# Kernel optimization log

Hardware: AMD Instinct MI355X
Metric: run time of the kernel (lower is better)

The kernel has to match this reference:

```python
import jax, jax.numpy as jnp
import numpy as np

B, T, S, H = 16, 1024, 1024, 512  # batch, dec len, src len, hidden


def setup_inputs() -> dict:
    key = jax.random.key(0)
    k1, k2, k3, k4 = jax.random.split(key, 4)
    decoder_output = jax.random.normal(k1, (B, T, H), dtype=jnp.float32)
    context = jax.random.normal(k2, (B, S, 2 * H), dtype=jnp.float32)
    mask = jax.random.randint(k3, (B, T, S), 0, 2) > 0  # bool
    # nn.Linear(2H, H, bias=False) weight: [H, 2H]
    W_a = jax.random.normal(k4, (H, 2 * H), dtype=jnp.float32) * (1.0 / np.sqrt(2 * H))
    return {"decoder_output": decoder_output, "context": context, "mask": mask, "W_a": W_a}


def reference(decoder_output, context, mask, W_a):
    # context_in = W_a(context).transpose(1, 2): [B, H, S]
    context_in = jnp.einsum('bsc,hc->bhs', context, W_a)
    # scores: [B, T, S]
    scores = jnp.einsum('bth,bhs->bts', decoder_output, context_in)
    scores = jnp.where(mask, jnp.float32(-1000000.0), scores)
    attn = jax.nn.softmax(scores, axis=2)
    # weighted sum over source: [B, T, 2H]
    weighted_sum = jnp.einsum('bts,bsc->btc', attn, context)
    return weighted_sum
```

## Files before the change

kernel.cpp:

```cpp
#include <hip/hip_runtime.h>
#include <cstdint>
#include <cstddef>


constexpr int BB = 16;
constexpr int TT = 1024;
constexpr int SS = 1024;
constexpr int HH = 512;

typedef __attribute__((ext_vector_type(8))) short short8v;
typedef __attribute__((ext_vector_type(4))) float f32x4;

__device__ inline unsigned short f2bf(float x) {
    unsigned int u = __float_as_uint(x);
    return (unsigned short)((u + 0x7FFFu + ((u >> 16) & 1u)) >> 16);
}
__device__ inline float bf2f(unsigned short h) {
    return __uint_as_float(((unsigned int)h) << 16);
}

__device__ inline void gload16(const void* g, void* l) {
    __builtin_amdgcn_global_load_lds(
        (const __attribute__((address_space(1))) unsigned int*)g,
        (__attribute__((address_space(3))) unsigned int*)l, 16, 0, 0);
}

__global__ __launch_bounds__(256)
void detect_mask(const unsigned char* __restrict__ mask, int* __restrict__ flag) {
    __shared__ int cnt;
    if (threadIdx.x == 0) cnt = 0;
    __syncthreads();
    int c = 0;
    for (int i = threadIdx.x; i < 4096; i += 256)
        if ((i & 3) != 0 && mask[i] != 0) c++;
    atomicAdd(&cnt, c);
    __syncthreads();
    if (threadIdx.x == 0) *flag = (cnt > 0) ? 1 : 0;
}

__global__ __launch_bounds__(256)
void split_hl(const float* __restrict__ in, unsigned short* __restrict__ oh,
              unsigned short* __restrict__ ol)
{
    const size_t i = ((size_t)blockIdx.x * 256 + threadIdx.x) * 8;
    const float4 x = *(const float4*)(in + i);
    const float4 y = *(const float4*)(in + i + 4);
    const float v[8] = {x.x, x.y, x.z, x.w, y.x, y.y, y.z, y.w};
    short8v H, L;
    #pragma unroll
    for (int j = 0; j < 8; ++j) {
        const unsigned short h = f2bf(v[j]);
        H[j] = (short)h;
        L[j] = (short)f2bf(v[j] - bf2f(h));
    }
    *(short8v*)(oh + i) = H;
    *(short8v*)(ol + i) = L;
}

__global__ __launch_bounds__(256)
void transpose_bf16(const float* __restrict__ src, unsigned short* __restrict__ dst,
                    long sS, long sD)
{
    __shared__ float t[32][33];
    const float*    s = src + (long)blockIdx.z * sS;
    unsigned short* d = dst + (long)blockIdx.z * sD;
    const int r0 = blockIdx.x << 5, c0 = blockIdx.y << 5;
    const int x = threadIdx.x & 31, y = threadIdx.x >> 5;
    #pragma unroll
    for (int i = 0; i < 32; i += 8)
        t[y + i][x] = s[(long)(r0 + y + i) * 1024 + c0 + x];
    __syncthreads();
    #pragma unroll
    for (int i = 0; i < 32; i += 8)
        d[(long)(c0 + y + i) * 1024 + r0 + x] = f2bf(t[x][y + i]);
}

template <bool SPLIT>
__global__ __launch_bounds__(256, 2)
void gemm_x3(const unsigned short* __restrict__ Ah, const unsigned short* __restrict__ Al,
             const unsigned short* __restrict__ Bh, const unsigned short* __restrict__ Bl,
             float* __restrict__ C, unsigned short* __restrict__ CH,
             unsigned short* __restrict__ CL,
             int N, int K, long sA, long sB, long sC)
{
    const int bz = blockIdx.z;
    Ah += (size_t)bz * sA;  Al += (size_t)bz * sA;
    Bh += (size_t)bz * sB;  Bl += (size_t)bz * sB;

    const int tid = threadIdx.x, lane = tid & 63, wv = tid >> 6;
    const int wr = wv >> 1, wc = wv & 1;
    const int m0 = blockIdx.x << 7, n0 = blockIdx.y << 7;

    __shared__ short sAh[8 * 512], sAl[8 * 512], sBh[8 * 512], sBl[8 * 512];

    const int r15 = lane & 15, k8 = (lane >> 4) << 3;
    const unsigned short* g;
    short* lw;
    if (wv == 0)      { g = Ah + (size_t)(m0 + r15) * K + k8; lw = sAh; }
    else if (wv == 1) { g = Al + (size_t)(m0 + r15) * K + k8; lw = sAl; }
    else if (wv == 2) { g = Bh + (size_t)(n0 + r15) * K + k8; lw = sBh; }
    else              { g = Bl + (size_t)(n0 + r15) * K + k8; lw = sBl; }

    f32x4 acc[4][4];
    #pragma unroll
    for (int i = 0; i < 4; ++i)
        #pragma unroll
        for (int j = 0; j < 4; ++j)
            acc[i][j] = (f32x4)(0.0f);

    for (int k0 = 0; k0 < K; k0 += 32) {
        __syncthreads();
        #pragma unroll
        for (int f = 0; f < 8; ++f)
            gload16(g + (size_t)f * 16 * K + k0, lw + f * 512);
        __syncthreads();

        short8v ah[4], al[4], bh[4], bl[4];
        #pragma unroll
        for (int f = 0; f < 4; ++f) {
            const int fa = (((wr << 2) + f) * 64 + lane) * 8;
            const int fb = (((wc << 2) + f) * 64 + lane) * 8;
            ah[f] = *(const short8v*)&sAh[fa];
            al[f] = *(const short8v*)&sAl[fa];
            bh[f] = *(const short8v*)&sBh[fb];
            bl[f] = *(const short8v*)&sBl[fb];
        }
        #pragma unroll
        for (int i = 0; i < 4; ++i)
            #pragma unroll
            for (int j = 0; j < 4; ++j) {
                acc[i][j] = __builtin_amdgcn_mfma_f32_16x16x32_bf16(ah[i], bh[j], acc[i][j], 0, 0, 0);
                acc[i][j] = __builtin_amdgcn_mfma_f32_16x16x32_bf16(ah[i], bl[j], acc[i][j], 0, 0, 0);
                acc[i][j] = __builtin_amdgcn_mfma_f32_16x16x32_bf16(al[i], bh[j], acc[i][j], 0, 0, 0);
            }
    }

    const int cr = (lane >> 4) << 2, cc = lane & 15;
    #pragma unroll
    for (int i = 0; i < 4; ++i) {
        const int row = m0 + (wr << 6) + (i << 4) + cr;
        #pragma unroll
        for (int j = 0; j < 4; ++j) {
            const int col = n0 + (wc << 6) + (j << 4) + cc;
            #pragma unroll
            for (int r = 0; r < 4; ++r) {
                const size_t idx = (size_t)bz * sC + (size_t)(row + r) * N + col;
                const float v = acc[i][j][r];
                if (SPLIT) {
                    const unsigned short h = f2bf(v);
                    CH[idx] = h;
                    CL[idx] = f2bf(v - bf2f(h));
                } else {
                    C[idx] = v;
                }
            }
        }
    }
}

__global__ __launch_bounds__(256, 2)
void gemm_x1(const unsigned short* __restrict__ A, const unsigned short* __restrict__ B,
             float* __restrict__ C, int N, int K, long sA, long sB, long sC)
{
    const int bz = blockIdx.z;
    A += (size_t)bz * sA;
    B += (size_t)bz * sB;

    const int tid = threadIdx.x, lane = tid & 63, wv = tid >> 6;
    const int wr = wv >> 1, wc = wv & 1;
    const int m0 = blockIdx.x << 7, n0 = blockIdx.y << 7;

    __shared__ short sA_[8 * 512], sB_[8 * 512];

    const int r15 = lane & 15, k8 = (lane >> 4) << 3;
    const int half = wv & 1;
    const unsigned short* g;
    short* lw;
    if (wv < 2) { g = A + (size_t)(m0 + (half << 6) + r15) * K + k8; lw = sA_ + (half << 2) * 512; }
    else        { g = B + (size_t)(n0 + (half << 6) + r15) * K + k8; lw = sB_ + (half << 2) * 512; }

    f32x4 acc[4][4];
    #pragma unroll
    for (int i = 0; i < 4; ++i)
        #pragma unroll
        for (int j = 0; j < 4; ++j)
            acc[i][j] = (f32x4)(0.0f);

    for (int k0 = 0; k0 < K; k0 += 32) {
        __syncthreads();
        #pragma unroll
        for (int f = 0; f < 4; ++f)
            gload16(g + (size_t)f * 16 * K + k0, lw + f * 512);
        __syncthreads();

        short8v a[4], b[4];
        #pragma unroll
        for (int f = 0; f < 4; ++f) {
            a[f] = *(const short8v*)&sA_[(((wr << 2) + f) * 64 + lane) * 8];
            b[f] = *(const short8v*)&sB_[(((wc << 2) + f) * 64 + lane) * 8];
        }
        #pragma unroll
        for (int i = 0; i < 4; ++i)
            #pragma unroll
            for (int j = 0; j < 4; ++j)
                acc[i][j] = __builtin_amdgcn_mfma_f32_16x16x32_bf16(a[i], b[j], acc[i][j], 0, 0, 0);
    }

    float* Cb = C + (size_t)bz * sC;
    const int cr = (lane >> 4) << 2, cc = lane & 15;
    #pragma unroll
    for (int i = 0; i < 4; ++i) {
        const int row = m0 + (wr << 6) + (i << 4) + cr;
        #pragma unroll
        for (int j = 0; j < 4; ++j) {
            const int col = n0 + (wc << 6) + (j << 4) + cc;
            #pragma unroll
            for (int r = 0; r < 4; ++r)
                Cb[(size_t)(row + r) * N + col] = acc[i][j][r];
        }
    }
}

__global__ __launch_bounds__(256)
void softmax_mask_bf16(const float* __restrict__ attnF, unsigned short* __restrict__ attnB,
                       const unsigned char* __restrict__ maskg,
                       const int* __restrict__ maskMode, long rowOff)
{
    __shared__ float red[8];
    const long row = blockIdx.x;
    const float4* p = (const float4*)(attnF + row * (long)SS);
    float4 v = p[threadIdx.x];

    const long mrow = (rowOff + row) * (long)SS;
    if (*maskMode) {
        const uchar4 mk = ((const uchar4*)(maskg + mrow))[threadIdx.x];
        if (mk.x) v.x = -1000000.0f;
        if (mk.y) v.y = -1000000.0f;
        if (mk.z) v.z = -1000000.0f;
        if (mk.w) v.w = -1000000.0f;
    } else {
        const int4 mk = ((const int4*)((const int*)maskg + mrow))[threadIdx.x];
        if (mk.x) v.x = -1000000.0f;
        if (mk.y) v.y = -1000000.0f;
        if (mk.z) v.z = -1000000.0f;
        if (mk.w) v.w = -1000000.0f;
    }

    float m = fmaxf(fmaxf(v.x, v.y), fmaxf(v.z, v.w));
    #pragma unroll
    for (int off = 32; off; off >>= 1)
        m = fmaxf(m, __shfl_xor(m, off));
    const int wave = threadIdx.x >> 6;
    if ((threadIdx.x & 63) == 0) red[wave] = m;
    __syncthreads();
    m = fmaxf(fmaxf(red[0], red[1]), fmaxf(red[2], red[3]));

    v.x = __expf(v.x - m);
    v.y = __expf(v.y - m);
    v.z = __expf(v.z - m);
    v.w = __expf(v.w - m);

    float s = v.x + v.y + v.z + v.w;
    #pragma unroll
    for (int off = 32; off; off >>= 1)
        s += __shfl_xor(s, off);
    if ((threadIdx.x & 63) == 0) red[4 + wave] = s;
    __syncthreads();
    s = red[4] + red[5] + red[6] + red[7];

    const float inv = 1.0f / s;
    ushort4 o;
    o.x = f2bf(v.x * inv);
    o.y = f2bf(v.y * inv);
    o.z = f2bf(v.z * inv);
    o.w = f2bf(v.w * inv);
    *(ushort4*)(attnB + row * (long)SS + 4 * threadIdx.x) = o;
}

extern "C" void kernel_launch(void* const* d_in, const int* in_sizes, int n_in,
                              void* d_out, int out_size, void* d_ws, size_t ws_size,
                              hipStream_t stream)
{
    const float*         dec  = (const float*)d_in[0];
    const float*         ctx  = (const float*)d_in[1];
    const unsigned char* mask = (const unsigned char*)d_in[2];
    const float*         Wa   = (const float*)d_in[3];
    float* out = (float*)d_out;

    const size_t MBy = 1u << 20;
    const size_t perBatch = 10 * MBy;
    const size_t fixed = 256 + 2 * MBy;
    int G = (ws_size > fixed) ? (int)((ws_size - fixed) / perBatch) : 1;
    if (G > BB) G = BB;
    if (G < 1)  G = 1;

    char* p = (char*)d_ws;
    int* maskMode = (int*)p;                 p += 256;
    unsigned short* WaH = (unsigned short*)p; p += (size_t)HH * 2 * HH * 2;
    unsigned short* WaL = (unsigned short*)p; p += (size_t)HH * 2 * HH * 2;
    unsigned short* ctxH = (unsigned short*)p;
    unsigned short* ctxL = ctxH + (size_t)G * SS * 2 * HH;
    float*          attnF = (float*)p;       p += (size_t)G * SS * 2 * HH * 4;
    unsigned short* cinH = (unsigned short*)p;
    unsigned short* cinL = cinH + (size_t)G * SS * HH;
    unsigned short* attnB = (unsigned short*)p;  p += (size_t)G * SS * HH * 2 * 2;
    unsigned short* decH = (unsigned short*)p;   p += (size_t)G * TT * HH * 2;
    unsigned short* decL = (unsigned short*)p;   p += (size_t)G * TT * HH * 2;
    unsigned short* ctxT = (unsigned short*)p;   p += (size_t)G * 2 * HH * SS * 2;

    detect_mask<<<1, 256, 0, stream>>>(mask, maskMode);
    split_hl<<<(HH * 2 * HH) / 2048, 256, 0, stream>>>(Wa, WaH, WaL);

    for (int g0 = 0; g0 < BB; g0 += G) {
        const int Gn = (BB - g0 < G) ? (BB - g0) : G;
        const float* ctxg = ctx + (size_t)g0 * SS * 2 * HH;

        split_hl<<<(Gn * SS * 2 * HH) / 2048, 256, 0, stream>>>(ctxg, ctxH, ctxL);
        split_hl<<<(Gn * TT * HH) / 2048, 256, 0, stream>>>(
            dec + (size_t)g0 * TT * HH, decH, decL);
        transpose_bf16<<<dim3(32, 32, Gn), 256, 0, stream>>>(
            ctxg, ctxT, (long)SS * 2 * HH, (long)2 * HH * SS);

        gemm_x3<true><<<dim3(SS / 128, HH / 128, Gn), 256, 0, stream>>>(
            ctxH, ctxL, WaH, WaL, nullptr, cinH, cinL,
            HH, 2 * HH, (long)SS * 2 * HH, 0L, (long)SS * HH);

        gemm_x3<false><<<dim3(TT / 128, SS / 128, Gn), 256, 0, stream>>>(
            decH, decL, cinH, cinL, attnF, nullptr, nullptr,
            SS, HH, (long)TT * HH, (long)SS * HH, (long)TT * SS);

        softmax_mask_bf16<<<Gn * TT, 256, 0, stream>>>(
            attnF, attnB, mask, maskMode, (long)g0 * TT);

        gemm_x1<<<dim3(TT / 128, (2 * HH) / 128, Gn), 256, 0, stream>>>(
            attnB, ctxT, out + (size_t)g0 * TT * 2 * HH,
            2 * HH, SS, (long)TT * SS, (long)2 * HH * SS, (long)TT * 2 * HH);
    }
}
```

Before: 456.0 us.

## Pre-pack GEMM operands into tile-contiguous layout and double-buffer LDS loads

Operands are repacked into 128x32 tile-contiguous blocks, either while splitting to bf16 hi/lo or in extra pack passes, so each GEMM k-step loads one contiguous 8 KB chunk per wave. The GEMM main loops now double-buffer LDS: the next tile's global-to-LDS load is issued before computing on the current one, which drops one barrier per iteration. The goal is to hide global load latency and get fully coalesced loads. The cost is extra pack kernels for cin and attn, more workspace per batch, and twice the LDS per block, which may reduce occupancy.

```diff
diff --git a/kernel.cpp b/kernel.cpp
--- a/kernel.cpp
+++ b/kernel.cpp
@@ -18,7 +18,6 @@
 __device__ inline float bf2f(unsigned short h) {
     return __uint_as_float(((unsigned int)h) << 16);
 }
-
 __device__ inline void gload16(const void* g, void* l) {
     __builtin_amdgcn_global_load_lds(
         (const __attribute__((address_space(1))) unsigned int*)g,
@@ -39,67 +38,106 @@
 }
 
 __global__ __launch_bounds__(256)
-void split_hl(const float* __restrict__ in, unsigned short* __restrict__ oh,
-              unsigned short* __restrict__ ol)
-{
-    const size_t i = ((size_t)blockIdx.x * 256 + threadIdx.x) * 8;
-    const float4 x = *(const float4*)(in + i);
-    const float4 y = *(const float4*)(in + i + 4);
-    const float v[8] = {x.x, x.y, x.z, x.w, y.x, y.y, y.z, y.w};
-    short8v H, L;
-    #pragma unroll
-    for (int j = 0; j < 8; ++j) {
-        const unsigned short h = f2bf(v[j]);
-        H[j] = (short)h;
-        L[j] = (short)f2bf(v[j] - bf2f(h));
-    }
-    *(short8v*)(oh + i) = H;
-    *(short8v*)(ol + i) = L;
+void split_pack(const float* __restrict__ in, unsigned short* __restrict__ oh,
+                unsigned short* __restrict__ ol, int K, int KT, long sIn, long sOut)
+{
+    in += (size_t)blockIdx.z * sIn;
+    oh += (size_t)blockIdx.z * sOut;
+    ol += (size_t)blockIdx.z * sOut;
+    const int rt = blockIdx.x / KT, kt = blockIdx.x % KT;
+    const size_t tileBase = (size_t)blockIdx.x * 4096;
+    #pragma unroll
+    for (int s = 0; s < 2; ++s) {
+        const int u  = threadIdx.x + (s << 8);
+        const int r  = ((u >> 6) << 4) + (u & 15);
+        const int k8 = ((u >> 4) & 3) << 3;
+        const float* src = in + (size_t)(rt * 128 + r) * K + kt * 32 + k8;
+        const float4 x = *(const float4*)src;
+        const float4 y = *(const float4*)(src + 4);
+        const float v[8] = {x.x, x.y, x.z, x.w, y.x, y.y, y.z, y.w};
+        short8v H, L;
+        #pragma unroll
+        for (int j = 0; j < 8; ++j) {
+            const unsigned short h = f2bf(v[j]);
+            H[j] = (short)h;
+            L[j] = (short)f2bf(v[j] - bf2f(h));
+        }
+        *(short8v*)(oh + tileBase + (size_t)u * 8) = H;
+        *(short8v*)(ol + tileBase + (size_t)u * 8) = L;
+    }
 }
 
 __global__ __launch_bounds__(256)
-void transpose_bf16(const float* __restrict__ src, unsigned short* __restrict__ dst,
-                    long sS, long sD)
-{
-    __shared__ float t[32][33];
-    const float*    s = src + (long)blockIdx.z * sS;
-    unsigned short* d = dst + (long)blockIdx.z * sD;
-    const int r0 = blockIdx.x << 5, c0 = blockIdx.y << 5;
-    const int x = threadIdx.x & 31, y = threadIdx.x >> 5;
-    #pragma unroll
-    for (int i = 0; i < 32; i += 8)
-        t[y + i][x] = s[(long)(r0 + y + i) * 1024 + c0 + x];
-    __syncthreads();
-    #pragma unroll
-    for (int i = 0; i < 32; i += 8)
-        d[(long)(c0 + y + i) * 1024 + r0 + x] = f2bf(t[x][y + i]);
+void pack_bf16(const unsigned short* __restrict__ in, unsigned short* __restrict__ op,
+               int K, int KT, long sIn, long sOut)
+{
+    in += (size_t)blockIdx.z * sIn;
+    op += (size_t)blockIdx.z * sOut;
+    const int rt = blockIdx.x / KT, kt = blockIdx.x % KT;
+    const size_t tileBase = (size_t)blockIdx.x * 4096;
+    #pragma unroll
+    for (int s = 0; s < 2; ++s) {
+        const int u  = threadIdx.x + (s << 8);
+        const int r  = ((u >> 6) << 4) + (u & 15);
+        const int k8 = ((u >> 4) & 3) << 3;
+        const short8v v = *(const short8v*)(in + (size_t)(rt * 128 + r) * K + kt * 32 + k8);
+        *(short8v*)(op + tileBase + (size_t)u * 8) = v;
+    }
+}
+
+__global__ __launch_bounds__(256)
+void transpose_pack(const float* __restrict__ src, unsigned short* __restrict__ dst,
+                    long sIn, long sOut)
+{
+    __shared__ float t[32][132];
+    src += (size_t)blockIdx.z * sIn;
+    dst += (size_t)blockIdx.z * sOut;
+    const int c0 = blockIdx.x << 7, s0 = blockIdx.y << 5;
+    #pragma unroll
+    for (int i = 0; i < 4; ++i) {
+        const int fl = threadIdx.x + (i << 8);
+        const int srow = fl >> 5, c4 = fl & 31;
+        const float4 v = *(const float4*)(src + (size_t)(s0 + srow) * (2 * HH) + c0 + (c4 << 2));
+        t[srow][(c4 << 2) + 0] = v.x;
+        t[srow][(c4 << 2) + 1] = v.y;
+        t[srow][(c4 << 2) + 2] = v.z;
+        t[srow][(c4 << 2) + 3] = v.w;
+    }
+    __syncthreads();
+    const size_t tileBase = ((size_t)blockIdx.x * (SS / 32) + blockIdx.y) * 4096;
+    #pragma unroll
+    for (int s = 0; s < 2; ++s) {
+        const int u = threadIdx.x + (s << 8);
+        const int r = ((u >> 6) << 4) + (u & 15);
+        const int o = (u >> 4) & 3;
+        short8v H;
+        #pragma unroll
+        for (int e = 0; e < 8; ++e)
+            H[e] = (short)f2bf(t[(o << 3) + e][r]);
+        *(short8v*)(dst + tileBase + (size_t)u * 8) = H;
+    }
 }
 
 template <bool SPLIT>
 __global__ __launch_bounds__(256, 2)
-void gemm_x3(const unsigned short* __restrict__ Ah, const unsigned short* __restrict__ Al,
-             const unsigned short* __restrict__ Bh, const unsigned short* __restrict__ Bl,
-             float* __restrict__ C, unsigned short* __restrict__ CH,
-             unsigned short* __restrict__ CL,
-             int N, int K, long sA, long sB, long sC)
+void gemm2_x3(const unsigned short* __restrict__ Ah, const unsigned short* __restrict__ Al,
+              const unsigned short* __restrict__ Bh, const unsigned short* __restrict__ Bl,
+              float* __restrict__ C, unsigned short* __restrict__ CH,
+              unsigned short* __restrict__ CL,
+              int N, int KTn, long sA, long sB, long sC)
 {
     const int bz = blockIdx.z;
-    Ah += (size_t)bz * sA;  Al += (size_t)bz * sA;
-    Bh += (size_t)bz * sB;  Bl += (size_t)bz * sB;
-
     const int tid = threadIdx.x, lane = tid & 63, wv = tid >> 6;
     const int wr = wv >> 1, wc = wv & 1;
-    const int m0 = blockIdx.x << 7, n0 = blockIdx.y << 7;
-
-    __shared__ short sAh[8 * 512], sAl[8 * 512], sBh[8 * 512], sBl[8 * 512];
-
-    const int r15 = lane & 15, k8 = (lane >> 4) << 3;
-    const unsigned short* g;
-    short* lw;
-    if (wv == 0)      { g = Ah + (size_t)(m0 + r15) * K + k8; lw = sAh; }
-    else if (wv == 1) { g = Al + (size_t)(m0 + r15) * K + k8; lw = sAl; }
-    else if (wv == 2) { g = Bh + (size_t)(n0 + r15) * K + k8; lw = sBh; }
-    else              { g = Bl + (size_t)(n0 + r15) * K + k8; lw = sBl; }
+    const int bx = blockIdx.x, by = blockIdx.y;
+
+    __shared__ short sm[2][4][4096];
+
+    const unsigned short* base =
+        (wv == 0) ? Ah + (size_t)bz * sA : (wv == 1) ? Al + (size_t)bz * sA
+      : (wv == 2) ? Bh + (size_t)bz * sB :            Bl + (size_t)bz * sB;
+    const unsigned short* gsrc = base
+        + (size_t)((wv < 2) ? bx : by) * KTn * 4096 + (size_t)lane * 8;
 
     f32x4 acc[4][4];
     #pragma unroll
@@ -108,22 +146,28 @@
         for (int j = 0; j < 4; ++j)
             acc[i][j] = (f32x4)(0.0f);
 
-    for (int k0 = 0; k0 < K; k0 += 32) {
-        __syncthreads();
-        #pragma unroll
-        for (int f = 0; f < 8; ++f)
-            gload16(g + (size_t)f * 16 * K + k0, lw + f * 512);
-        __syncthreads();
-
+    #pragma unroll
+    for (int f = 0; f < 8; ++f)
+        gload16(gsrc + f * 512, &sm[0][wv][f * 512]);
+    __syncthreads();
+
+    int cur = 0;
+    for (int kt = 0; kt < KTn; ++kt) {
+        if (kt + 1 < KTn) {
+            const unsigned short* g = gsrc + (size_t)(kt + 1) * 4096;
+            #pragma unroll
+            for (int f = 0; f < 8; ++f)
+                gload16(g + f * 512, &sm[cur ^ 1][wv][f * 512]);
+        }
         short8v ah[4], al[4], bh[4], bl[4];
         #pragma unroll
         for (int f = 0; f < 4; ++f) {
             const int fa = (((wr << 2) + f) * 64 + lane) * 8;
             const int fb = (((wc << 2) + f) * 64 + lane) * 8;
-            ah[f] = *(const short8v*)&sAh[fa];
-            al[f] = *(const short8v*)&sAl[fa];
-            bh[f] = *(const short8v*)&sBh[fb];
-            bl[f] = *(const short8v*)&sBl[fb];
+            ah[f] = *(const short8v*)&sm[cur][0][fa];
+            al[f] = *(const short8v*)&sm[cur][1][fa];
+            bh[f] = *(const short8v*)&sm[cur][2][fb];
+            bl[f] = *(const short8v*)&sm[cur][3][fb];
         }
         #pragma unroll
         for (int i = 0; i < 4; ++i)
@@ -133,15 +177,17 @@
                 acc[i][j] = __builtin_amdgcn_mfma_f32_16x16x32_bf16(ah[i], bl[j], acc[i][j], 0, 0, 0);
                 acc[i][j] = __builtin_amdgcn_mfma_f32_16x16x32_bf16(al[i], bh[j], acc[i][j], 0, 0, 0);
             }
+        __syncthreads();
+        cur ^= 1;
     }
 
     const int cr = (lane >> 4) << 2, cc = lane & 15;
     #pragma unroll
     for (int i = 0; i < 4; ++i) {
-        const int row = m0 + (wr << 6) + (i << 4) + cr;
+        const int row = (bx << 7) + (wr << 6) + (i << 4) + cr;
         #pragma unroll
         for (int j = 0; j < 4; ++j) {
-            const int col = n0 + (wc << 6) + (j << 4) + cc;
+            const int col = (by << 7) + (wc << 6) + (j << 4) + cc;
             #pragma unroll
             for (int r = 0; r < 4; ++r) {
                 const size_t idx = (size_t)bz * sC + (size_t)(row + r) * N + col;
@@ -159,25 +205,22 @@
 }
 
 __global__ __launch_bounds__(256, 2)
-void gemm_x1(const unsigned short* __restrict__ A, const unsigned short* __restrict__ B,
-             float* __restrict__ C, int N, int K, long sA, long sB, long sC)
+void gemm2_x1(const unsigned short* __restrict__ A, const unsigned short* __restrict__ B,
+              float* __restrict__ C, int N, int KTn, long sA, long sB, long sC)
 {
     const int bz = blockIdx.z;
-    A += (size_t)bz * sA;
-    B += (size_t)bz * sB;
-
     const int tid = threadIdx.x, lane = tid & 63, wv = tid >> 6;
     const int wr = wv >> 1, wc = wv & 1;
-    const int m0 = blockIdx.x << 7, n0 = blockIdx.y << 7;
-
-    __shared__ short sA_[8 * 512], sB_[8 * 512];
-
-    const int r15 = lane & 15, k8 = (lane >> 4) << 3;
+    const int bx = blockIdx.x, by = blockIdx.y;
+
+    __shared__ short sm[2][2][4096];
+
     const int half = wv & 1;
-    const unsigned short* g;
-    short* lw;
-    if (wv < 2) { g = A + (size_t)(m0 + (half << 6) + r15) * K + k8; lw = sA_ + (half << 2) * 512; }
-    else        { g = B + (size_t)(n0 + (half << 6) + r15) * K + k8; lw = sB_ + (half << 2) * 512; }
+    const unsigned short* base = (wv < 2) ? A + (size_t)bz * sA : B + (size_t)bz * sB;
+    const unsigned short* gsrc = base
+        + (size_t)((wv < 2) ? bx : by) * KTn * 4096 + (size_t)(half * 4) * 512
+        + (size_t)lane * 8;
+    short* ldst = &sm[0][wv < 2 ? 0 : 1][half * 2048];
 
     f32x4 acc[4][4];
     #pragma unroll
@@ -186,34 +229,43 @@
         for (int j = 0; j < 4; ++j)
             acc[i][j] = (f32x4)(0.0f);
 
-    for (int k0 = 0; k0 < K; k0 += 32) {
-        __syncthreads();
-        #pragma unroll
-        for (int f = 0; f < 4; ++f)
-            gload16(g + (size_t)f * 16 * K + k0, lw + f * 512);
-        __syncthreads();
-
+    #pragma unroll
+    for (int f = 0; f < 4; ++f)
+        gload16(gsrc + f * 512, ldst + f * 512);
+    __syncthreads();
+
+    int cur = 0;
+    for (int kt = 0; kt < KTn; ++kt) {
+        if (kt + 1 < KTn) {
+            const unsigned short* g = gsrc + (size_t)(kt + 1) * 4096;
+            short* l = &sm[cur ^ 1][wv < 2 ? 0 : 1][half * 2048];
+            #pragma unroll
+            for (int f = 0; f < 4; ++f)
+                gload16(g + f * 512, l + f * 512);
+        }
         short8v a[4], b[4];
         #pragma unroll
         for (int f = 0; f < 4; ++f) {
-            a[f] = *(const short8v*)&sA_[(((wr << 2) + f) * 64 + lane) * 8];
-            b[f] = *(const short8v*)&sB_[(((wc << 2) + f) * 64 + lane) * 8];
+            a[f] = *(const short8v*)&sm[cur][0][(((wr << 2) + f) * 64 + lane) * 8];
+            b[f] = *(const short8v*)&sm[cur][1][(((wc << 2) + f) * 64 + lane) * 8];
         }
         #pragma unroll
         for (int i = 0; i < 4; ++i)
             #pragma unroll
             for (int j = 0; j < 4; ++j)
                 acc[i][j] = __builtin_amdgcn_mfma_f32_16x16x32_bf16(a[i], b[j], acc[i][j], 0, 0, 0);
+        __syncthreads();
+        cur ^= 1;
     }
 
     float* Cb = C + (size_t)bz * sC;
     const int cr = (lane >> 4) << 2, cc = lane & 15;
     #pragma unroll
     for (int i = 0; i < 4; ++i) {
-        const int row = m0 + (wr << 6) + (i << 4) + cr;
+        const int row = (bx << 7) + (wr << 6) + (i << 4) + cr;
         #pragma unroll
         for (int j = 0; j < 4; ++j) {
-            const int col = n0 + (wc << 6) + (j << 4) + cc;
+            const int col = (by << 7) + (wc << 6) + (j << 4) + cc;
             #pragma unroll
             for (int r = 0; r < 4; ++r)
                 Cb[(size_t)(row + r) * N + col] = acc[i][j][r];
@@ -288,52 +340,66 @@
     float* out = (float*)d_out;
 
     const size_t MBy = 1u << 20;
-    const size_t perBatch = 10 * MBy;
+    const size_t perBatch = 12 * MBy;
     const size_t fixed = 256 + 2 * MBy;
     int G = (ws_size > fixed) ? (int)((ws_size - fixed) / perBatch) : 1;
     if (G > BB) G = BB;
     if (G < 1)  G = 1;
 
     char* p = (char*)d_ws;
-    int* maskMode = (int*)p;                 p += 256;
-    unsigned short* WaH = (unsigned short*)p; p += (size_t)HH * 2 * HH * 2;
-    unsigned short* WaL = (unsigned short*)p; p += (size_t)HH * 2 * HH * 2;
-    unsigned short* ctxH = (unsigned short*)p;
-    unsigned short* ctxL = ctxH + (size_t)G * SS * 2 * HH;
-    float*          attnF = (float*)p;       p += (size_t)G * SS * 2 * HH * 4;
-    unsigned short* cinH = (unsigned short*)p;
-    unsigned short* cinL = cinH + (size_t)G * SS * HH;
-    unsigned short* attnB = (unsigned short*)p;  p += (size_t)G * SS * HH * 2 * 2;
-    unsigned short* decH = (unsigned short*)p;   p += (size_t)G * TT * HH * 2;
-    unsigned short* decL = (unsigned short*)p;   p += (size_t)G * TT * HH * 2;
-    unsigned short* ctxT = (unsigned short*)p;   p += (size_t)G * 2 * HH * SS * 2;
+    int* maskMode = (int*)p;                      p += 256;
+    unsigned short* WaHP = (unsigned short*)p;    p += (size_t)HH * 2 * HH * 2;
+    unsigned short* WaLP = (unsigned short*)p;    p += (size_t)HH * 2 * HH * 2;
+    unsigned short* ctxHP = (unsigned short*)p;
+    unsigned short* ctxLP = ctxHP + (size_t)G * SS * 2 * HH;
+    float*          attnF = (float*)p;            p += (size_t)G * 4 * MBy;
+    unsigned short* decHP = (unsigned short*)p;
+    unsigned short* decLP = decHP + (size_t)G * TT * HH;
+    unsigned short* attnB = (unsigned short*)p;   p += (size_t)G * 2 * MBy;
+    unsigned short* cinH  = (unsigned short*)p;
+    unsigned short* cinL  = cinH + (size_t)G * SS * HH;
+    unsigned short* attnP = (unsigned short*)p;   p += (size_t)G * 2 * MBy;
+    unsigned short* cinHP = (unsigned short*)p;
+    unsigned short* cinLP = cinHP + (size_t)G * SS * HH;  p += (size_t)G * 2 * MBy;
+    unsigned short* ctxTP = (unsigned short*)p;   p += (size_t)G * 2 * MBy;
 
     detect_mask<<<1, 256, 0, stream>>>(mask, maskMode);
-    split_hl<<<(HH * 2 * HH) / 2048, 256, 0, stream>>>(Wa, WaH, WaL);
+    split_pack<<<dim3(4 * 32, 1, 1), 256, 0, stream>>>(
+        Wa, WaHP, WaLP, 2 * HH, 32, 0L, 0L);
 
     for (int g0 = 0; g0 < BB; g0 += G) {
         const int Gn = (BB - g0 < G) ? (BB - g0) : G;
         const float* ctxg = ctx + (size_t)g0 * SS * 2 * HH;
 
-        split_hl<<<(Gn * SS * 2 * HH) / 2048, 256, 0, stream>>>(ctxg, ctxH, ctxL);
-        split_hl<<<(Gn * TT * HH) / 2048, 256, 0, stream>>>(
-            dec + (size_t)g0 * TT * HH, decH, decL);
-        transpose_bf16<<<dim3(32, 32, Gn), 256, 0, stream>>>(
-            ctxg, ctxT, (long)SS * 2 * HH, (long)2 * HH * SS);
-
-        gemm_x3<true><<<dim3(SS / 128, HH / 128, Gn), 256, 0, stream>>>(
-            ctxH, ctxL, WaH, WaL, nullptr, cinH, cinL,
-            HH, 2 * HH, (long)SS * 2 * HH, 0L, (long)SS * HH);
-
-        gemm_x3<false><<<dim3(TT / 128, SS / 128, Gn), 256, 0, stream>>>(
-            decH, decL, cinH, cinL, attnF, nullptr, nullptr,
-            SS, HH, (long)TT * HH, (long)SS * HH, (long)TT * SS);
+        split_pack<<<dim3(8 * 32, 1, Gn), 256, 0, stream>>>(
+            ctxg, ctxHP, ctxLP, 2 * HH, 32, (long)SS * 2 * HH, (long)SS * 2 * HH);
+        split_pack<<<dim3(8 * 16, 1, Gn), 256, 0, stream>>>(
+            dec + (size_t)g0 * TT * HH, decHP, decLP, HH, 16,
+            (long)TT * HH, (long)TT * HH);
+        transpose_pack<<<dim3(8, 32, Gn), 256, 0, stream>>>(
+            ctxg, ctxTP, (long)SS * 2 * HH, (long)2 * HH * SS);
+
+        gemm2_x3<true><<<dim3(8, 4, Gn), 256, 0, stream>>>(
+            ctxHP, ctxLP, WaHP, WaLP, nullptr, cinH, cinL,
+            HH, 32, (long)SS * 2 * HH, 0L, (long)SS * HH);
+
+        pack_bf16<<<dim3(8 * 16, 1, Gn), 256, 0, stream>>>(
+            cinH, cinHP, HH, 16, (long)SS * HH, (long)SS * HH);
+        pack_bf16<<<dim3(8 * 16, 1, Gn), 256, 0, stream>>>(
+            cinL, cinLP, HH, 16, (long)SS * HH, (long)SS * HH);
+
+        gemm2_x3<false><<<dim3(8, 8, Gn), 256, 0, stream>>>(
+            decHP, decLP, cinHP, cinLP, attnF, nullptr, nullptr,
+            SS, 16, (long)TT * HH, (long)SS * HH, (long)TT * SS);
 
         softmax_mask_bf16<<<Gn * TT, 256, 0, stream>>>(
             attnF, attnB, mask, maskMode, (long)g0 * TT);
 
-        gemm_x1<<<dim3(TT / 128, (2 * HH) / 128, Gn), 256, 0, stream>>>(
-            attnB, ctxT, out + (size_t)g0 * TT * 2 * HH,
-            2 * HH, SS, (long)TT * SS, (long)2 * HH * SS, (long)TT * 2 * HH);
-    }
-}
+        pack_bf16<<<dim3(8 * 32, 1, Gn), 256, 0, stream>>>(
+            attnB, attnP, SS, 32, (long)TT * SS, (long)TT * SS);
+
+        gemm2_x1<<<dim3(8, 8, Gn), 256, 0, stream>>>(
+            attnP, ctxTP, out + (size_t)g0 * TT * 2 * HH,
+            2 * HH, 32, (long)TT * SS, (long)2 * HH * SS, (long)TT * 2 * HH);
+    }
+}
```

Result: faster. 433.9 us (-4.9%).
